# Optimization experiments

Hardware: AMD Instinct MI355X
Metric: run time of the kernel (lower is better)

The kernel has to match this reference:

```python
import jax, jax.numpy as jnp
import numpy as np
from jax import lax

BETA = 0.1
N_CLUSTERS = 64


def setup_inputs() -> dict:
    key = jax.random.key(0)
    ks = jax.random.split(key, 10)
    L, B, Hin, H = 200, 2048, 64, 256
    s = lambda k, shape, scale=0.05: jax.random.normal(k, shape, dtype=jnp.float32) * scale
    return {
        "X": jax.random.normal(ks[0], (L, B, Hin), dtype=jnp.float32),
        "W_ih0": s(ks[1], (4 * H, Hin)),
        "W_hh0": s(ks[2], (4 * H, H)),
        "b_ih0": s(ks[3], (4 * H,)),
        "b_hh0": s(ks[4], (4 * H,)),
        "W_ih1": s(ks[5], (4 * H, H)),
        "W_hh1": s(ks[6], (4 * H, H)),
        "b_ih1": s(ks[7], (4 * H,)),
        "b_hh1": s(ks[8], (4 * H,)),
        "clusters": jax.random.normal(ks[9], (N_CLUSTERS, H), dtype=jnp.float32),
    }


def _lstm_layer(x, W_ih, W_hh, b_ih, b_hh):
    # x: (L, B, I) -> outputs (L, B, H); torch gate order i, f, g, o
    H = W_hh.shape[1]
    B = x.shape[1]
    b = b_ih + b_hh

    def step(carry, xt):
        h, c = carry
        gates = xt @ W_ih.T + h @ W_hh.T + b  # (B, 4H)
        i, f, g, o = jnp.split(gates, 4, axis=-1)
        c = jax.nn.sigmoid(f) * c + jax.nn.sigmoid(i) * jnp.tanh(g)
        h = jax.nn.sigmoid(o) * jnp.tanh(c)
        return (h, c), h

    h0 = jnp.zeros((B, H), x.dtype)
    (_, _), ys = lax.scan(step, (h0, h0), x)
    return ys


def _encode(X, W_ih0, W_hh0, b_ih0, b_hh0, W_ih1, W_hh1, b_ih1, b_hh1):
    y0 = _lstm_layer(X, W_ih0, W_hh0, b_ih0, b_hh0)
    y1 = _lstm_layer(y0, W_ih1, W_hh1, b_ih1, b_hh1)
    return y1[-1]  # latent_X: (B, H), last timestep of top layer


def reference(X, W_ih0, W_hh0, b_ih0, b_hh0, W_ih1, W_hh1, b_ih1, b_hh1, clusters):
    latent_X = _encode(X, W_ih0, W_hh0, b_ih0, b_hh0, W_ih1, W_hh1, b_ih1, b_hh1)

    # kmeans assignment on detached latents (l2 distance)
    lat_sg = lax.stop_gradient(latent_X)
    d2 = (jnp.sum(lat_sg * lat_sg, -1, keepdims=True)
          - 2.0 * lat_sg @ clusters.T
          + jnp.sum(clusters * clusters, -1))  # (B, K)
    cluster_id = jnp.argmin(d2, axis=-1)  # (B,)

    # centroid update from assigned (detached) points; keep old centroid if empty
    sums = jax.ops.segment_sum(lat_sg, cluster_id, num_segments=N_CLUSTERS)
    counts = jax.ops.segment_sum(jnp.ones((lat_sg.shape[0],), lat_sg.dtype),
                                 cluster_id, num_segments=N_CLUSTERS)
    upd = jnp.where(counts[:, None] > 0, sums / jnp.maximum(counts, 1.0)[:, None], clusters)

    # vectorized per-sample cluster distance loss: sum_i 0.5*beta*||latent_i - c[id_i]||^2
    diff = latent_X - upd[cluster_id]  # gather (B, H)
    dist_loss = 0.5 * BETA * jnp.sum(diff * diff)
    return latent_X, dist_loss
```

## Files before the change

### kernel.cpp

```cpp
#include <hip/hip_runtime.h>
#include <hip/hip_bf16.h>
#include <math.h>

typedef unsigned short u16;
typedef unsigned int u32;
typedef __attribute__((ext_vector_type(8))) __bf16 bf16x8;
typedef __attribute__((ext_vector_type(4))) float f32x4;

#define LSTM_L 200
#define LSTM_B 2048
#define LSTM_HIN 64
#define LSTM_H 256
#define NCLUST 64
#define HALF_BETA 0.05f
#define LDS_BYTES 131072

__device__ __forceinline__ void gload_lds16(const void* g, void* l) {
    __builtin_amdgcn_global_load_lds(
        (__attribute__((address_space(1))) const void*)g,
        (__attribute__((address_space(3))) void*)l, 16, 0, 0);
}

__device__ __forceinline__ float fast_sigmoid(float x) {
    return __builtin_amdgcn_rcpf(1.f + __expf(-x));
}
__device__ __forceinline__ float fast_tanh(float x) {
    return 2.f * __builtin_amdgcn_rcpf(1.f + __expf(-2.f * x)) - 1.f;
}

template<int KIN>
__global__ __launch_bounds__(256) void pack_frag(
    const float* __restrict__ Wih, const float* __restrict__ Whh,
    u16* __restrict__ Wp)
{
    constexpr int NCH = (KIN + LSTM_H) / 32;
    const int total = 1024 * (KIN + LSTM_H);
    for (int i = blockIdx.x * 256 + threadIdx.x; i < total; i += gridDim.x * 256) {
        const int e = i & 7;
        int t = i >> 3;
        const int lane = t & 63; t >>= 6;
        const int nf = t & 1;    t >>= 1;
        const int ch = t % NCH;  t /= NCH;
        const int wn = t & 3;
        const int nb = t >> 2;
        const int l15 = lane & 15;
        const int j = (2 * nf + (l15 & 1)) * 256 + nb * 32 + wn * 8 + (l15 >> 1);
        const int k = ch * 32 + ((lane >> 4) << 3) + e;
        const float v = (k < KIN) ? Wih[(size_t)j * KIN + k]
                                  : Whh[(size_t)j * LSTM_H + (k - KIN)];
        Wp[i] = __builtin_bit_cast(u16, (__bf16)v);
    }
}

template<int KIN>
__device__ __forceinline__ void run_layer(
    const float* __restrict__ xf32,
    const u16* __restrict__ hbelow,
    const u16* __restrict__ hself,
    const u16* __restrict__ Wp,
    const float* __restrict__ bih, const float* __restrict__ bhh,
    u16* __restrict__ hout, float* __restrict__ latout,
    float* __restrict__ cst,
    int blk, char* smem, int tid)
{
    constexpr int NCH = (KIN + LSTM_H) / 32;
    constexpr bool IS_L0 = (KIN == 64);
    const int lane = tid & 63;
    const int w = tid >> 6;
    const int wm = w >> 2;
    const int wn = w & 3;
    const int l15 = lane & 15;
    const int q = lane >> 4;
    const int mb = blk >> 3;
    const int nb = blk & 7;
    const int b0 = mb * 128;

    bf16x8 Breg[NCH][2];
    {
        const u16* wp = Wp + (size_t)((nb * 4 + wn) * NCH) * 1024 + lane * 8;
#pragma unroll
        for (int ch = 0; ch < NCH; ++ch)
#pragma unroll
            for (int nf = 0; nf < 2; ++nf)
                Breg[ch][nf] = *(const bf16x8*)(wp + (ch * 2 + nf) * 512);
    }

    const int hcol = nb * 32 + wn * 8 + (l15 >> 1);
    const int rowA = wm * 64;
    float cp[4][4];
#pragma unroll
    for (int mf = 0; mf < 4; ++mf)
#pragma unroll
        for (int r = 0; r < 4; ++r)
            cp[mf][r] = cst[(size_t)(b0 + rowA + mf * 16 + q * 4 + r) * 256 + hcol];

    const int gpar = l15 & 1;
    const float b0a = bih[gpar * 256 + hcol] + bhh[gpar * 256 + hcol];
    const float b1a = bih[(2 + gpar) * 256 + hcol] + bhh[(2 + gpar) * 256 + hcol];

    if (IS_L0) {
#pragma unroll
        for (int i = 0; i < 8; ++i) {
            const int slot = i * 512 + tid;
            const int row = slot >> 5;
            const int so = (slot & 31) * 16;
            const int koff = so ^ ((row & 7) << 4);
            gload_lds16((const char*)hself + (size_t)(b0 + row) * 512 + koff,
                        smem + slot * 16);
        }
#pragma unroll
        for (int p = 0; p < 2; ++p) {
            const int slot = p * 512 + tid;
            const int row = slot >> 3;
            const int so = (slot & 7) * 16;
            const int koff = so ^ ((row & 7) << 4);
            const float* s = xf32 + (size_t)(b0 + row) * 64 + (koff >> 1);
            const float4 v0 = *(const float4*)s;
            const float4 v1 = *(const float4*)(s + 4);
            bf16x8 pk;
            pk[0] = (__bf16)v0.x; pk[1] = (__bf16)v0.y;
            pk[2] = (__bf16)v0.z; pk[3] = (__bf16)v0.w;
            pk[4] = (__bf16)v1.x; pk[5] = (__bf16)v1.y;
            pk[6] = (__bf16)v1.z; pk[7] = (__bf16)v1.w;
            *(bf16x8*)(smem + 65536 + slot * 16) = pk;
        }
    } else {
#pragma unroll
        for (int i = 0; i < 16; ++i) {
            const int slot = i * 512 + tid;
            const int row = slot >> 6;
            const int so = (slot & 63) * 16;
            const int koff = so ^ ((row & 7) << 4);
            const char* src = (koff < 512)
                ? (const char*)hbelow + (size_t)(b0 + row) * 512 + koff
                : (const char*)hself + (size_t)(b0 + row) * 512 + (koff - 512);
            gload_lds16(src, smem + slot * 16);
        }
    }
    __syncthreads();

    f32x4 acc[4][2];
#pragma unroll
    for (int mf = 0; mf < 4; ++mf)
#pragma unroll
        for (int nf = 0; nf < 2; ++nf) acc[mf][nf] = f32x4{0.f, 0.f, 0.f, 0.f};

    const int qoff = q * 16;
    const int swzl = (l15 & 7) << 4;
#pragma unroll
    for (int ch = 0; ch < NCH; ++ch) {
        bf16x8 af[4];
#pragma unroll
        for (int mf = 0; mf < 4; ++mf) {
            const int row = rowA + mf * 16 + l15;
            const char* ap;
            if (IS_L0) {
                if (ch < 2)
                    ap = smem + 65536 + row * 128 + ((ch * 64 + qoff) ^ swzl);
                else
                    ap = smem + row * 512 + (((ch - 2) * 64 + qoff) ^ swzl);
            } else {
                ap = smem + row * 1024 + ((ch * 64 + qoff) ^ swzl);
            }
            af[mf] = *(const bf16x8*)ap;
        }
#pragma unroll
        for (int mf = 0; mf < 4; ++mf)
#pragma unroll
            for (int nf = 0; nf < 2; ++nf)
                acc[mf][nf] = __builtin_amdgcn_mfma_f32_16x16x32_bf16(
                    af[mf], Breg[ch][nf], acc[mf][nf], 0, 0, 0);
    }

#pragma unroll
    for (int mf = 0; mf < 4; ++mf) {
#pragma unroll
        for (int r = 0; r < 4; ++r) {
            const float a0 = acc[mf][0][r] + b0a;
            const float a1 = acc[mf][1][r] + b1a;
            const float p0 = __shfl_xor(a0, 1);
            const float p1 = __shfl_xor(a1, 1);
            const float gi = gpar ? p0 : a0;
            const float gf = gpar ? a0 : p0;
            const float gg = gpar ? p1 : a1;
            const float go = gpar ? a1 : p1;
            const float cn = fast_sigmoid(gf) * cp[mf][r]
                           + fast_sigmoid(gi) * fast_tanh(gg);
            const float hv = fast_sigmoid(go) * fast_tanh(cn);
            const size_t oidx =
                (size_t)(b0 + rowA + mf * 16 + q * 4 + r) * 256 + hcol;
            if (gpar) {
                cst[oidx] = cn;
            } else if (latout) {
                latout[oidx] = hv;
            } else {
                hout[oidx] = __builtin_bit_cast(u16, (__bf16)hv);
            }
        }
    }
}

__global__ __launch_bounds__(512, 1) void lstm_slot(
    const float* __restrict__ xt,
    const u16* __restrict__ h0c, u16* __restrict__ h0n, float* __restrict__ c0,
    const u16* __restrict__ Wp0,
    const float* __restrict__ bih0, const float* __restrict__ bhh0,
    const u16* __restrict__ h1c, u16* __restrict__ h1n, float* __restrict__ c1,
    const u16* __restrict__ Wp1,
    const float* __restrict__ bih1, const float* __restrict__ bhh1,
    float* __restrict__ latout, int do0, int do1)
{
    extern __shared__ char smem[];
    const int tid = threadIdx.x;
    if (blockIdx.x < 128) {
        if (do0)
            run_layer<LSTM_HIN>(xt, nullptr, h0c, Wp0, bih0, bhh0,
                                h0n, nullptr, c0, blockIdx.x, smem, tid);
    } else {
        if (do1)
            run_layer<LSTM_H>(nullptr, h0c, h1c, Wp1, bih1, bhh1,
                              h1n, latout, c1, blockIdx.x - 128, smem, tid);
    }
}

__global__ __launch_bounds__(64) void assign_accum(
    const float* __restrict__ lat, const float* __restrict__ clusters,
    int* __restrict__ ids, float* __restrict__ sums, int* __restrict__ counts)
{
    __shared__ float row[LSTM_H];
    const int b = blockIdx.x;
    const int k = threadIdx.x;
    for (int i = k; i < LSTM_H; i += 64) row[i] = lat[(size_t)b * LSTM_H + i];
    __syncthreads();
    const float* ck = clusters + (size_t)k * LSTM_H;
    float d = 0.f;
#pragma unroll 8
    for (int i = 0; i < LSTM_H; ++i) { const float t = row[i] - ck[i]; d += t * t; }
    int idx = k;
    for (int off = 32; off > 0; off >>= 1) {
        const float od = __shfl_down(d, off, 64);
        const int   oi = __shfl_down(idx, off, 64);
        if (od < d || (od == d && oi < idx)) { d = od; idx = oi; }
    }
    const int best = __shfl(idx, 0, 64);
    if (k == 0) { ids[b] = best; atomicAdd(&counts[best], 1); }
#pragma unroll
    for (int j = 0; j < 4; ++j)
        atomicAdd(&sums[(size_t)best * LSTM_H + k * 4 + j], row[k * 4 + j]);
}

__global__ __launch_bounds__(256) void centroid_final(
    const float* __restrict__ sums, const int* __restrict__ counts,
    const float* __restrict__ clusters, float* __restrict__ upd)
{
    const int k = blockIdx.x;
    const int h = threadIdx.x;
    const int c = counts[k];
    upd[(size_t)k * LSTM_H + h] = (c > 0)
        ? sums[(size_t)k * LSTM_H + h] / (float)c
        : clusters[(size_t)k * LSTM_H + h];
}

__global__ __launch_bounds__(256) void loss_kernel(
    const float* __restrict__ lat, const int* __restrict__ ids,
    const float* __restrict__ upd, float* __restrict__ out_loss)
{
    float p = 0.f;
    const int total = LSTM_B * LSTM_H;
    for (int idx = blockIdx.x * blockDim.x + threadIdx.x; idx < total;
         idx += gridDim.x * blockDim.x) {
        const int b = idx >> 8;
        const float d = lat[idx] - upd[(size_t)ids[b] * LSTM_H + (idx & 255)];
        p += d * d;
    }
    for (int off = 32; off > 0; off >>= 1) p += __shfl_down(p, off, 64);
    __shared__ float wsum[4];
    const int lane = threadIdx.x & 63, wid = threadIdx.x >> 6;
    if (lane == 0) wsum[wid] = p;
    __syncthreads();
    if (threadIdx.x == 0)
        atomicAdd(out_loss, HALF_BETA * (wsum[0] + wsum[1] + wsum[2] + wsum[3]));
}

extern "C" void kernel_launch(void* const* d_in, const int* in_sizes, int n_in,
                              void* d_out, int out_size, void* d_ws, size_t ws_size,
                              hipStream_t stream)
{
    const float* X     = (const float*)d_in[0];
    const float* Wih0  = (const float*)d_in[1];
    const float* Whh0  = (const float*)d_in[2];
    const float* bih0  = (const float*)d_in[3];
    const float* bhh0  = (const float*)d_in[4];
    const float* Wih1  = (const float*)d_in[5];
    const float* Whh1  = (const float*)d_in[6];
    const float* bih1  = (const float*)d_in[7];
    const float* bhh1  = (const float*)d_in[8];
    const float* clust = (const float*)d_in[9];

    float* out = (float*)d_out;
    char* base = (char*)d_ws;
    const size_t MB = 1u << 20;
    const size_t KB = 1024;

    u16* Wp0    = (u16*)(base + 0 * MB);
    u16* Wp1    = (u16*)(base + 1 * MB);
    u16* h0a    = (u16*)(base + 2 * MB);
    u16* h0b    = (u16*)(base + 3 * MB);
    u16* h1a    = (u16*)(base + 4 * MB);
    u16* h1b    = (u16*)(base + 5 * MB);
    float* c0   = (float*)(base + 6 * MB);
    float* c1   = (float*)(base + 8 * MB);
    float* sums = (float*)(base + 10 * MB);
    float* upd  = (float*)(base + 10 * MB + 64 * KB);
    int* counts = (int*)(base + 10 * MB + 128 * KB);
    int* ids    = (int*)(base + 10 * MB + 132 * KB);

    const size_t BH = (size_t)LSTM_B * LSTM_H;

    hipMemsetAsync(h0a, 0, MB, stream);
    hipMemsetAsync(h1a, 0, MB, stream);
    hipMemsetAsync(c0, 0, 4 * MB, stream);
    hipMemsetAsync(base + 10 * MB, 0, 144 * KB, stream);
    hipMemsetAsync(out + BH, 0, sizeof(float), stream);

    pack_frag<LSTM_HIN><<<320, 256, 0, stream>>>(Wih0, Whh0, Wp0);
    pack_frag<LSTM_H>  <<<512, 256, 0, stream>>>(Wih1, Whh1, Wp1);

    hipFuncSetAttribute((const void*)lstm_slot,
                        hipFuncAttributeMaxDynamicSharedMemorySize, LDS_BYTES);

    u16* h0c = h0a; u16* h0n = h0b;
    u16* h1c = h1a; u16* h1n = h1b;
    for (int s = 0; s <= LSTM_L; ++s) {
        const int do0 = (s < LSTM_L) ? 1 : 0;
        const int do1 = (s > 0) ? 1 : 0;
        const float* xt = do0 ? X + (size_t)s * LSTM_B * LSTM_HIN : nullptr;
        float* lat = (s == LSTM_L) ? out : nullptr;
        lstm_slot<<<256, 512, LDS_BYTES, stream>>>(
            xt, h0c, h0n, c0, Wp0, bih0, bhh0,
            h1c, h1n, c1, Wp1, bih1, bhh1, lat, do0, do1);
        if (do0) { u16* t = h0c; h0c = h0n; h0n = t; }
        if (do1) { u16* t = h1c; h1c = h1n; h1n = t; }
    }

    assign_accum<<<LSTM_B, 64, 0, stream>>>(out, clust, ids, sums, counts);
    centroid_final<<<NCLUST, 256, 0, stream>>>(sums, counts, clust, upd);
    loss_kernel<<<256, 256, 0, stream>>>(out, ids, upd, out + BH);
}
```

Before: 2.817 ms.

## Pack bf16 h stores into 32-bit writes and restructure k-means assignment with LDS partials

In the LSTM epilogue, neighbouring bf16 hidden values are exchanged with a lane shuffle so one lane writes a packed 32-bit word, and all stores use relaxed agent-scope atomic stores. Separately, the k-means assignment is rewritten: 32 blocks each stage a transposed copy of the clusters in LDS, accumulate per-block sums and counts in LDS, and write partials that a new final kernel reduces. This removes the global atomics and the zeroing memset, but limits the assignment phase to 32 blocks.

```diff
diff --git a/kernel.cpp b/kernel.cpp
--- a/kernel.cpp
+++ b/kernel.cpp
@@ -14,6 +14,8 @@
 #define NCLUST 64
 #define HALF_BETA 0.05f
 #define LDS_BYTES 131072
+#define ASSIGN_LDS 135424
+#define ASSIGN_BLOCKS 32
 
 __device__ __forceinline__ void gload_lds16(const void* g, void* l) {
     __builtin_amdgcn_global_load_lds(
@@ -26,6 +28,9 @@
 }
 __device__ __forceinline__ float fast_tanh(float x) {
     return 2.f * __builtin_amdgcn_rcpf(1.f + __expf(-2.f * x)) - 1.f;
+}
+__device__ __forceinline__ void wt_store(u32* p, u32 v) {
+    __hip_atomic_store(p, v, __ATOMIC_RELAXED, __HIP_MEMORY_SCOPE_AGENT);
 }
 
 template<int KIN>
@@ -187,14 +192,17 @@
             const float cn = fast_sigmoid(gf) * cp[mf][r]
                            + fast_sigmoid(gi) * fast_tanh(gg);
             const float hv = fast_sigmoid(go) * fast_tanh(cn);
-            const size_t oidx =
-                (size_t)(b0 + rowA + mf * 16 + q * 4 + r) * 256 + hcol;
+            const int rowo = b0 + rowA + mf * 16 + q * 4 + r;
+            const size_t oidx = (size_t)rowo * 256 + hcol;
+            const u16 hb = __builtin_bit_cast(u16, (__bf16)hv);
+            const int pr = __shfl_xor((int)(u32)hb, 2);
+            const u32 pk = ((u32)hb & 0xffffu) | (((u32)pr) << 16);
             if (gpar) {
-                cst[oidx] = cn;
+                wt_store((u32*)&cst[oidx], __builtin_bit_cast(u32, cn));
             } else if (latout) {
-                latout[oidx] = hv;
-            } else {
-                hout[oidx] = __builtin_bit_cast(u16, (__bf16)hv);
+                wt_store((u32*)&latout[oidx], __builtin_bit_cast(u32, hv));
+            } else if ((l15 & 3) == 0) {
+                wt_store((u32*)hout + ((size_t)rowo * 128 + (hcol >> 1)), pk);
             }
         }
     }
@@ -223,41 +231,73 @@
     }
 }
 
-__global__ __launch_bounds__(64) void assign_accum(
+__global__ __launch_bounds__(256, 1) void assign_fused(
     const float* __restrict__ lat, const float* __restrict__ clusters,
-    int* __restrict__ ids, float* __restrict__ sums, int* __restrict__ counts)
-{
-    __shared__ float row[LSTM_H];
-    const int b = blockIdx.x;
-    const int k = threadIdx.x;
-    for (int i = k; i < LSTM_H; i += 64) row[i] = lat[(size_t)b * LSTM_H + i];
+    int* __restrict__ ids, float* __restrict__ partial, int* __restrict__ pcount)
+{
+    extern __shared__ char sm[];
+    float* clT    = (float*)sm;
+    float* psum   = (float*)(sm + 65536);
+    float* rowbuf = (float*)(sm + 131072);
+    int*   pcnt   = (int*)(sm + 135168);
+
+    const int tid = threadIdx.x;
+    const int k = tid & 63;
+    const int w = tid >> 6;
+
+    for (int i = tid; i < 16384; i += 256) {
+        const int kk = i >> 8, j = i & 255;
+        clT[j * 64 + kk] = clusters[(size_t)kk * 256 + j];
+        psum[i] = 0.f;
+    }
+    if (tid < 64) pcnt[tid] = 0;
     __syncthreads();
-    const float* ck = clusters + (size_t)k * LSTM_H;
-    float d = 0.f;
+
+    float* rb = rowbuf + w * 256;
+    const int rbase = (int)blockIdx.x * 64 + w * 16;
+    for (int rr = 0; rr < 16; ++rr) {
+        const int row = rbase + rr;
+#pragma unroll
+        for (int p = 0; p < 4; ++p)
+            rb[p * 64 + k] = lat[(size_t)row * 256 + p * 64 + k];
+        float d = 0.f;
 #pragma unroll 8
-    for (int i = 0; i < LSTM_H; ++i) { const float t = row[i] - ck[i]; d += t * t; }
-    int idx = k;
-    for (int off = 32; off > 0; off >>= 1) {
-        const float od = __shfl_down(d, off, 64);
-        const int   oi = __shfl_down(idx, off, 64);
-        if (od < d || (od == d && oi < idx)) { d = od; idx = oi; }
-    }
-    const int best = __shfl(idx, 0, 64);
-    if (k == 0) { ids[b] = best; atomicAdd(&counts[best], 1); }
-#pragma unroll
-    for (int j = 0; j < 4; ++j)
-        atomicAdd(&sums[(size_t)best * LSTM_H + k * 4 + j], row[k * 4 + j]);
-}
-
-__global__ __launch_bounds__(256) void centroid_final(
-    const float* __restrict__ sums, const int* __restrict__ counts,
+        for (int j = 0; j < 256; ++j) {
+            const float t = rb[j] - clT[j * 64 + k];
+            d += t * t;
+        }
+        int idx = k;
+        for (int off = 32; off > 0; off >>= 1) {
+            const float od = __shfl_down(d, off, 64);
+            const int   oi = __shfl_down(idx, off, 64);
+            if (od < d || (od == d && oi < idx)) { d = od; idx = oi; }
+        }
+        const int best = __shfl(idx, 0, 64);
+        if (k == 0) { ids[row] = best; atomicAdd(&pcnt[best], 1); }
+#pragma unroll
+        for (int p = 0; p < 4; ++p)
+            atomicAdd(&psum[best * 256 + p * 64 + k], rb[p * 64 + k]);
+    }
+    __syncthreads();
+    for (int i = tid; i < 16384; i += 256)
+        partial[(size_t)blockIdx.x * 16384 + i] = psum[i];
+    if (tid < 64) pcount[(size_t)blockIdx.x * 64 + tid] = pcnt[tid];
+}
+
+__global__ __launch_bounds__(256) void centroid_final2(
+    const float* __restrict__ partial, const int* __restrict__ pcount,
     const float* __restrict__ clusters, float* __restrict__ upd)
 {
     const int k = blockIdx.x;
     const int h = threadIdx.x;
-    const int c = counts[k];
+    float s = 0.f;
+    int c = 0;
+    for (int b = 0; b < ASSIGN_BLOCKS; ++b) {
+        s += partial[(size_t)b * 16384 + k * 256 + h];
+        c += pcount[(size_t)b * 64 + k];
+    }
     upd[(size_t)k * LSTM_H + h] = (c > 0)
-        ? sums[(size_t)k * LSTM_H + h] / (float)c
+        ? s / (float)c
         : clusters[(size_t)k * LSTM_H + h];
 }
 
@@ -302,25 +342,24 @@
     const size_t MB = 1u << 20;
     const size_t KB = 1024;
 
-    u16* Wp0    = (u16*)(base + 0 * MB);
-    u16* Wp1    = (u16*)(base + 1 * MB);
-    u16* h0a    = (u16*)(base + 2 * MB);
-    u16* h0b    = (u16*)(base + 3 * MB);
-    u16* h1a    = (u16*)(base + 4 * MB);
-    u16* h1b    = (u16*)(base + 5 * MB);
-    float* c0   = (float*)(base + 6 * MB);
-    float* c1   = (float*)(base + 8 * MB);
-    float* sums = (float*)(base + 10 * MB);
-    float* upd  = (float*)(base + 10 * MB + 64 * KB);
-    int* counts = (int*)(base + 10 * MB + 128 * KB);
-    int* ids    = (int*)(base + 10 * MB + 132 * KB);
+    u16* Wp0      = (u16*)(base + 0 * MB);
+    u16* Wp1      = (u16*)(base + 1 * MB);
+    u16* h0a      = (u16*)(base + 2 * MB);
+    u16* h0b      = (u16*)(base + 3 * MB);
+    u16* h1a      = (u16*)(base + 4 * MB);
+    u16* h1b      = (u16*)(base + 5 * MB);
+    float* c0     = (float*)(base + 6 * MB);
+    float* c1     = (float*)(base + 8 * MB);
+    float* partial= (float*)(base + 10 * MB);
+    float* upd    = (float*)(base + 12 * MB);
+    int* pcount   = (int*)(base + 12 * MB + 64 * KB);
+    int* ids      = (int*)(base + 12 * MB + 72 * KB);
 
     const size_t BH = (size_t)LSTM_B * LSTM_H;
 
     hipMemsetAsync(h0a, 0, MB, stream);
     hipMemsetAsync(h1a, 0, MB, stream);
     hipMemsetAsync(c0, 0, 4 * MB, stream);
-    hipMemsetAsync(base + 10 * MB, 0, 144 * KB, stream);
     hipMemsetAsync(out + BH, 0, sizeof(float), stream);
 
     pack_frag<LSTM_HIN><<<320, 256, 0, stream>>>(Wih0, Whh0, Wp0);
@@ -328,6 +367,8 @@
 
     hipFuncSetAttribute((const void*)lstm_slot,
                         hipFuncAttributeMaxDynamicSharedMemorySize, LDS_BYTES);
+    hipFuncSetAttribute((const void*)assign_fused,
+                        hipFuncAttributeMaxDynamicSharedMemorySize, ASSIGN_LDS);
 
     u16* h0c = h0a; u16* h0n = h0b;
     u16* h1c = h1a; u16* h1n = h1b;
@@ -343,7 +384,8 @@
         if (do1) { u16* t = h1c; h1c = h1n; h1n = t; }
     }
 
-    assign_accum<<<LSTM_B, 64, 0, stream>>>(out, clust, ids, sums, counts);
-    centroid_final<<<NCLUST, 256, 0, stream>>>(sums, counts, clust, upd);
+    assign_fused<<<ASSIGN_BLOCKS, 256, ASSIGN_LDS, stream>>>(
+        out, clust, ids, partial, pcount);
+    centroid_final2<<<NCLUST, 256, 0, stream>>>(partial, pcount, clust, upd);
     loss_kernel<<<256, 256, 0, stream>>>(out, ids, upd, out + BH);
 }
```

Result: faster. 2.655 ms (-5.7%).
